# Kernel optimization log

Hardware: AMD Instinct MI355X
Metric: run time of the kernel (lower is better)

Reference implementation:

```python
import jax, jax.numpy as jnp
import numpy as np

N = 100000   # nodes
E = 1600000  # edges (no self loops; added per PyG default)
DIN = 64; DMID = 64; DOUT = 64; H = 8
C_MID = DMID // H  # per-head dim for concat layers
NEG_SLOPE = 0.2


def _segment_softmax(logits, seg, num):
    # logits: [E', H], seg: [E'] target node ids
    m = jax.ops.segment_max(logits, seg, num_segments=num)  # [N, H]
    e = jnp.exp(logits - m[seg])
    s = jax.ops.segment_sum(e, seg, num_segments=num)
    return e / (s[seg] + 1e-16)


def _gatv2_layer(x, src, dst, Wl, Wr, att, bias, heads, concat):
    n = x.shape[0]
    c = Wl.shape[1] // heads
    xl = (x @ Wl).reshape(n, heads, c)  # source transform
    xr = (x @ Wr).reshape(n, heads, c)  # target transform
    m = xl[src] + xr[dst]               # [E', H, C] gathered messages
    e = jnp.where(m > 0, m, NEG_SLOPE * m)
    alpha = jnp.einsum('ehc,hc->eh', e, att)            # [E', H]
    alpha = _segment_softmax(alpha, dst, n)
    out = jax.ops.segment_sum(alpha[..., None] * xl[src], dst, num_segments=n)  # [N, H, C]
    if concat:
        out = out.reshape(n, heads * c)
    else:
        out = out.mean(axis=1)
    return out + bias


def setup_inputs() -> dict:
    key = jax.random.key(0)
    ks = jax.random.split(key, 16)
    x = jax.random.normal(ks[0], (N, DIN), jnp.float32)
    src = jax.random.randint(ks[1], (E,), 0, N)
    dst = jax.random.randint(ks[2], (E,), 0, N)
    dst = jnp.where(src == dst, (dst + 1) % N, dst)  # no pre-existing self loops
    edge_index = jnp.stack([src, dst]).astype(jnp.int64)

    def lin(k, fi, fo):
        return jax.random.normal(k, (fi, fo), jnp.float32) / np.sqrt(fi)

    inp = {'x': x, 'edge_index': edge_index}
    # layer 0: din -> H*C_MID (concat), layer 1: dmid -> H*C_MID (concat), layer 2: dmid -> H*DOUT (mean)
    dims = [(DIN, H * C_MID, C_MID), (DMID, H * C_MID, C_MID), (DMID, H * DOUT, DOUT)]
    kidx = 3
    for i, (fi, fo, c) in enumerate(dims):
        inp[f'W{i}l'] = lin(ks[kidx], fi, fo); kidx += 1
        inp[f'W{i}r'] = lin(ks[kidx], fi, fo); kidx += 1
        inp[f'a{i}'] = jax.random.normal(ks[kidx], (H, c), jnp.float32) / np.sqrt(c); kidx += 1
        bsize = fo if i < 2 else DOUT
        inp[f'b{i}'] = jnp.zeros((bsize,), jnp.float32)
    return inp


def reference(x, edge_index, W0l, W0r, a0, b0, W1l, W1r, a1, b1, W2l, W2r, a2, b2):
    # add self loops (PyG GATv2Conv default add_self_loops=True)
    loop = jnp.arange(N, dtype=edge_index.dtype)
    src = jnp.concatenate([edge_index[0], loop])
    dst = jnp.concatenate([edge_index[1], loop])

    # eval mode: dropout is identity
    h = jax.nn.elu(_gatv2_layer(x, src, dst, W0l, W0r, a0, b0, H, True))
    prev_h = jnp.zeros_like(h)

    h_in = h + prev_h
    h = jax.nn.elu(_gatv2_layer(h_in, src, dst, W1l, W1r, a1, b1, H, True))
    prev_h = h_in

    h_in = h + prev_h
    out = _gatv2_layer(h_in, src, dst, W2l, W2r, a2, b2, H, False)
    return out
```

## Files before the change

kernel.cpp:

```cpp
#include <hip/hip_runtime.h>
#include <math.h>

#define NNODES 100000
typedef unsigned short bf16_t;

typedef __attribute__((ext_vector_type(8))) short bf16x8;
typedef __attribute__((ext_vector_type(4))) float f32x4;

__device__ __forceinline__ float bf_lo(unsigned u) { return __uint_as_float(u << 16); }
__device__ __forceinline__ float bf_hi(unsigned u) { return __uint_as_float(u & 0xffff0000u); }
__device__ __forceinline__ bf16_t f2bf(float f) {
  unsigned u = __float_as_uint(f);
  return (bf16_t)((u + 0x7fffu + ((u >> 16) & 1u)) >> 16);
}
__device__ __forceinline__ float leaky(float v) { return fmaxf(v, 0.2f * v); }

#define LDK 68

__global__ __launch_bounds__(256) void gemm_mfma(const float* __restrict__ in,
                                                 const float* __restrict__ Wl,
                                                 const float* __restrict__ Wr,
                                                 bf16_t* __restrict__ XL,
                                                 bf16_t* __restrict__ XR,
                                                 int n, int fo, int col0, int ncols) {
  __shared__ bf16_t sX[64][LDK];
  __shared__ bf16_t sL[64][LDK];
  __shared__ bf16_t sR[64][LDK];
  int r0 = blockIdx.x * 64;
  int ct = blockIdx.y * 64;
  for (int i = threadIdx.x; i < 64 * 64; i += 256) {
    int r = i >> 6, k = i & 63;
    float v = (r0 + r < n) ? in[(size_t)(r0 + r) * 64 + k] : 0.f;
    sX[r][k] = f2bf(v);
  }
  for (int i = threadIdx.x; i < 64 * 64; i += 256) {
    int k = i >> 6, c = i & 63;
    int gc = col0 + ct + c;
    sL[c][k] = f2bf(Wl[k * fo + gc]);
    sR[c][k] = f2bf(Wr[k * fo + gc]);
  }
  __syncthreads();
  int w = threadIdx.x >> 6, l = threadIdx.x & 63;
  int l16 = l & 15, kg = l >> 4;
  bf16x8 a0 = *(const bf16x8*)&sX[w * 16 + l16][kg * 8];
  bf16x8 a1 = *(const bf16x8*)&sX[w * 16 + l16][kg * 8 + 32];
  f32x4 accL[4], accR[4];
#pragma unroll
  for (int nt = 0; nt < 4; ++nt) {
#pragma unroll
    for (int r = 0; r < 4; ++r) { accL[nt][r] = 0.f; accR[nt][r] = 0.f; }
  }
#pragma unroll
  for (int nt = 0; nt < 4; ++nt) {
    bf16x8 bl0 = *(const bf16x8*)&sL[nt * 16 + l16][kg * 8];
    bf16x8 bl1 = *(const bf16x8*)&sL[nt * 16 + l16][kg * 8 + 32];
    bf16x8 br0 = *(const bf16x8*)&sR[nt * 16 + l16][kg * 8];
    bf16x8 br1 = *(const bf16x8*)&sR[nt * 16 + l16][kg * 8 + 32];
    accL[nt] = __builtin_amdgcn_mfma_f32_16x16x32_bf16(a0, bl0, accL[nt], 0, 0, 0);
    accL[nt] = __builtin_amdgcn_mfma_f32_16x16x32_bf16(a1, bl1, accL[nt], 0, 0, 0);
    accR[nt] = __builtin_amdgcn_mfma_f32_16x16x32_bf16(a0, br0, accR[nt], 0, 0, 0);
    accR[nt] = __builtin_amdgcn_mfma_f32_16x16x32_bf16(a1, br1, accR[nt], 0, 0, 0);
  }
#pragma unroll
  for (int nt = 0; nt < 4; ++nt) {
#pragma unroll
    for (int r = 0; r < 4; ++r) {
      int grow = r0 + w * 16 + kg * 4 + r;
      if (grow < n) {
        size_t o = (size_t)grow * ncols + ct + nt * 16 + l16;
        XL[o] = f2bf(accL[nt][r]);
        XR[o] = f2bf(accR[nt][r]);
      }
    }
  }
}

__global__ void zeroi(int* __restrict__ p, int n) {
  int i = blockIdx.x * blockDim.x + threadIdx.x;
  if (i < n) p[i] = 0;
}
__global__ void histrank(const int* __restrict__ ei, int E,
                         int* __restrict__ cnt, unsigned char* __restrict__ rank) {
  int e = blockIdx.x * blockDim.x + threadIdx.x;
  if (e < E) rank[e] = (unsigned char)atomicAdd(&cnt[ei[E + e]], 1);
}
__global__ void scan1(const int* __restrict__ cnt, int n,
                      int* __restrict__ scn, int* __restrict__ bsum) {
  __shared__ int sh[256];
  int t = threadIdx.x, i = blockIdx.x * 256 + t;
  int v = (i < n) ? cnt[i] : 0;
  sh[t] = v;
  __syncthreads();
  for (int off = 1; off < 256; off <<= 1) {
    int x = (t >= off) ? sh[t - off] : 0;
    __syncthreads();
    sh[t] += x;
    __syncthreads();
  }
  if (i < n) scn[i] = sh[t];
  if (t == 255) bsum[blockIdx.x] = sh[255];
}
__global__ void scan2(int* __restrict__ bsum, int nb) {
  __shared__ int sh[512];
  int t = threadIdx.x;
  sh[t] = (t < nb) ? bsum[t] : 0;
  __syncthreads();
  for (int off = 1; off < 512; off <<= 1) {
    int x = (t >= off) ? sh[t - off] : 0;
    __syncthreads();
    sh[t] += x;
    __syncthreads();
  }
  if (t < nb) bsum[t] = sh[t];
}
__global__ void scan3(int* __restrict__ RS, const int* __restrict__ bsum, int n) {
  int i = blockIdx.x * blockDim.x + threadIdx.x;
  if (i >= n) return;
  int b = i >> 8;
  int pre = (b > 0) ? bsum[b - 1] : 0;
  RS[i + 1] += pre;
  if (i == 0) RS[0] = 0;
}
__global__ void scat2(const int* __restrict__ ei, int E,
                      const int* __restrict__ RS,
                      const unsigned char* __restrict__ rank,
                      int* __restrict__ SRC) {
  int e = blockIdx.x * blockDim.x + threadIdx.x;
  if (e >= E) return;
  int d = ei[E + e];
  SRC[RS[d] + (int)rank[e]] = ei[e];
}

__global__ __launch_bounds__(256) void fused01(const bf16_t* __restrict__ xl,
                                               const bf16_t* __restrict__ xr,
                                               const float* __restrict__ att,
                                               const int* __restrict__ RS,
                                               const int* __restrict__ SRC,
                                               const float* __restrict__ bias,
                                               float* __restrict__ curbuf,
                                               int n, int addres) {
  int l = threadIdx.x & 63;
  int q = l & 15;
  int d = blockIdx.x * 16 + ((threadIdx.x >> 6) << 2) + (l >> 4);
  int dd = (d < n) ? d : 0;
  float a0 = att[4 * q], a1 = att[4 * q + 1], a2 = att[4 * q + 2], a3 = att[4 * q + 3];
  uint2 ur = ((const uint2*)xr)[(size_t)dd * 16 + q];
  float r0 = bf_lo(ur.x), r1 = bf_hi(ur.x), r2 = bf_lo(ur.y), r3 = bf_hi(ur.y);
  int rs = RS[dd], re = RS[dd + 1];
  int cnt = (d < n) ? (re - rs + 1) : 0;
  int mc = max(cnt, __shfl_xor(cnt, 16));
  mc = max(mc, __shfl_xor(mc, 32));
  float m = -1e30f, s = 0.f, ac0 = 0.f, ac1 = 0.f, ac2 = 0.f, ac3 = 0.f;
  int nsid = (rs < re) ? SRC[rs] : dd;
  uint2 u = ((const uint2*)xl)[(size_t)dd * 16 + q];
  for (int j = 0;;) {
    uint2 un = ((const uint2*)xl)[(size_t)nsid * 16 + q];
    int i2 = rs + j + 1;
    int nn = (i2 < re) ? SRC[i2] : dd;
    float x0 = bf_lo(u.x), x1 = bf_hi(u.x), x2 = bf_lo(u.y), x3 = bf_hi(u.y);
    float t = leaky(x0 + r0) * a0 + leaky(x1 + r1) * a1 +
              leaky(x2 + r2) * a2 + leaky(x3 + r3) * a3;
    t += __shfl_xor(t, 1);
    if (j >= cnt) t = -1e30f;
    if (__any(t > m + 8.f)) {
      float nm = fmaxf(m, t);
      float e0 = __expf(m - nm);
      s *= e0; ac0 *= e0; ac1 *= e0; ac2 *= e0; ac3 *= e0; m = nm;
    }
    float e1 = __expf(t - m);
    s += e1;
    ac0 += e1 * x0; ac1 += e1 * x1; ac2 += e1 * x2; ac3 += e1 * x3;
    ++j;
    if (j >= mc) break;
    u = un;
    nsid = nn;
  }
  if (d < n) {
    float inv = 1.f / (s + 1e-16f);
    float v0 = ac0 * inv + bias[4 * q];
    float v1 = ac1 * inv + bias[4 * q + 1];
    float v2 = ac2 * inv + bias[4 * q + 2];
    float v3 = ac3 * inv + bias[4 * q + 3];
    v0 = v0 > 0.f ? v0 : expm1f(v0);
    v1 = v1 > 0.f ? v1 : expm1f(v1);
    v2 = v2 > 0.f ? v2 : expm1f(v2);
    v3 = v3 > 0.f ? v3 : expm1f(v3);
    float4* pc = (float4*)(curbuf + (size_t)d * 64 + 4 * q);
    if (addres) {
      float4 pr = *pc;
      v0 += pr.x; v1 += pr.y; v2 += pr.z; v3 += pr.w;
    }
    *pc = make_float4(v0, v1, v2, v3);
  }
}

__global__ __launch_bounds__(256) void fused2(const bf16_t* __restrict__ xl,
                                              const bf16_t* __restrict__ xr,
                                              const float* __restrict__ att,
                                              const int* __restrict__ RS,
                                              const int* __restrict__ SRC,
                                              const float* __restrict__ bias,
                                              float* __restrict__ accbuf,
                                              float* __restrict__ outbuf,
                                              int n, int h0, int pass) {
  int l = threadIdx.x & 63;
  int ll = l & 31;
  int d = blockIdx.x * 8 + ((threadIdx.x >> 6) << 1) + (l >> 5);
  int dd = (d < n) ? d : 0;
  int h = ll >> 3, c0 = (ll & 7) * 8;
  const float* ap = att + (h0 + h) * 64 + c0;
  float a[8];
#pragma unroll
  for (int k = 0; k < 8; ++k) a[k] = ap[k];
  uint4 ur = ((const uint4*)xr)[(size_t)dd * 32 + ll];
  float r[8] = {bf_lo(ur.x), bf_hi(ur.x), bf_lo(ur.y), bf_hi(ur.y),
                bf_lo(ur.z), bf_hi(ur.z), bf_lo(ur.w), bf_hi(ur.w)};
  int rs = RS[dd], re = RS[dd + 1];
  int cnt = (d < n) ? (re - rs + 1) : 0;
  int maxcnt = max(cnt, __shfl_xor(cnt, 32));
  float m = -1e30f, s = 0.f;
  float ac[8] = {0.f, 0.f, 0.f, 0.f, 0.f, 0.f, 0.f, 0.f};
  int nsid = (rs < re) ? SRC[rs] : dd;
  uint4 u = ((const uint4*)xl)[(size_t)dd * 32 + ll];
  for (int j = 0;;) {
    uint4 un = ((const uint4*)xl)[(size_t)nsid * 32 + ll];
    int i2 = rs + j + 1;
    int nn = (i2 < re) ? SRC[i2] : dd;
    float x[8] = {bf_lo(u.x), bf_hi(u.x), bf_lo(u.y), bf_hi(u.y),
                  bf_lo(u.z), bf_hi(u.z), bf_lo(u.w), bf_hi(u.w)};
    float t = 0.f;
#pragma unroll
    for (int k = 0; k < 8; ++k) t += leaky(x[k] + r[k]) * a[k];
    t += __shfl_xor(t, 1);
    t += __shfl_xor(t, 2);
    t += __shfl_xor(t, 4);
    if (j >= cnt) t = -1e30f;
    if (__any(t > m + 8.f)) {
      float nm = fmaxf(m, t);
      float e0 = __expf(m - nm);
      s *= e0;
#pragma unroll
      for (int k = 0; k < 8; ++k) ac[k] *= e0;
      m = nm;
    }
    float e1 = __expf(t - m);
    s += e1;
#pragma unroll
    for (int k = 0; k < 8; ++k) ac[k] += e1 * x[k];
    ++j;
    if (j >= maxcnt) break;
    u = un;
    nsid = nn;
  }
  float inv = 1.f / (s + 1e-16f);
  float v[8];
#pragma unroll
  for (int k = 0; k < 8; ++k) {
    v[k] = ac[k] * inv;
    v[k] += __shfl_xor(v[k], 8);
    v[k] += __shfl_xor(v[k], 16);
  }
  if (ll < 8 && d < n) {
    float* pa = accbuf + (size_t)d * 64 + ll * 8;
    if (pass == 0) {
      *(float4*)pa = make_float4(v[0], v[1], v[2], v[3]);
      *(float4*)(pa + 4) = make_float4(v[4], v[5], v[6], v[7]);
    } else {
      float4 p0 = *(float4*)pa;
      float4 p1 = *(float4*)(pa + 4);
      const float* bp = bias + ll * 8;
      float4 o0, o1;
      o0.x = (p0.x + v[0]) * 0.125f + bp[0];
      o0.y = (p0.y + v[1]) * 0.125f + bp[1];
      o0.z = (p0.z + v[2]) * 0.125f + bp[2];
      o0.w = (p0.w + v[3]) * 0.125f + bp[3];
      o1.x = (p1.x + v[4]) * 0.125f + bp[4];
      o1.y = (p1.y + v[5]) * 0.125f + bp[5];
      o1.z = (p1.z + v[6]) * 0.125f + bp[6];
      o1.w = (p1.w + v[7]) * 0.125f + bp[7];
      float* po = outbuf + (size_t)d * 64 + ll * 8;
      *(float4*)po = o0;
      *(float4*)(po + 4) = o1;
    }
  }
}

extern "C" void kernel_launch(void* const* d_in, const int* in_sizes, int n_in,
                              void* d_out, int out_size, void* d_ws, size_t ws_size,
                              hipStream_t stream) {
  const float* x = (const float*)d_in[0];
  const int* ei = (const int*)d_in[1];
  const float* Wmat[3][2] = {
      {(const float*)d_in[2], (const float*)d_in[3]},
      {(const float*)d_in[6], (const float*)d_in[7]},
      {(const float*)d_in[10], (const float*)d_in[11]}};
  const float* att[3] = {(const float*)d_in[4], (const float*)d_in[8],
                         (const float*)d_in[12]};
  const float* bias[3] = {(const float*)d_in[5], (const float*)d_in[9],
                          (const float*)d_in[13]};
  const int N = NNODES;
  int E = in_sizes[1] / 2;

  char* p = (char*)d_ws;
  auto alloc = [&](size_t bytes) {
    char* r = p;
    p += (bytes + 255) & ~(size_t)255;
    return r;
  };
  float* CUR = (float*)alloc((size_t)N * 64 * 4);
  float* ACC = (float*)alloc((size_t)N * 64 * 4);
  bf16_t* XL = (bf16_t*)alloc((size_t)N * 256 * 2);
  bf16_t* XR = (bf16_t*)alloc((size_t)N * 256 * 2);
  int* RS = (int*)alloc((size_t)(N + 1) * 4);
  int* CNT = (int*)alloc((size_t)N * 4);
  int* BSUM = (int*)alloc(512 * 4);
  int* SRC = (int*)alloc((size_t)E * 4);
  unsigned char* RANK = (unsigned char*)alloc((size_t)E);

  const int nb = (N + 255) / 256;
  const int geblk = (E + 255) / 256;
  const int g01 = (N + 15) / 16;
  const int g2 = (N + 7) / 8;
  const int gx64 = (N + 63) / 64;

  zeroi<<<nb, 256, 0, stream>>>(CNT, N);
  histrank<<<geblk, 256, 0, stream>>>(ei, E, CNT, RANK);
  scan1<<<nb, 256, 0, stream>>>(CNT, N, RS + 1, BSUM);
  scan2<<<1, 512, 0, stream>>>(BSUM, nb);
  scan3<<<nb, 256, 0, stream>>>(RS, BSUM, N);
  scat2<<<geblk, 256, 0, stream>>>(ei, E, RS, RANK, SRC);

  for (int layer = 0; layer < 2; ++layer) {
    const float* in = (layer == 0) ? x : CUR;
    gemm_mfma<<<dim3(gx64, 1), 256, 0, stream>>>(in, Wmat[layer][0], Wmat[layer][1],
                                                 XL, XR, N, 64, 0, 64);
    fused01<<<g01, 256, 0, stream>>>(XL, XR, att[layer], RS, SRC, bias[layer],
                                     CUR, N, layer);
  }

  for (int hb = 0; hb < 2; ++hb) {
    gemm_mfma<<<dim3(gx64, 4), 256, 0, stream>>>(CUR, Wmat[2][0], Wmat[2][1],
                                                 XL, XR, N, 512, hb * 256, 256);
    fused2<<<g2, 256, 0, stream>>>(XL, XR, att[2], RS, SRC, bias[2],
                                   ACC, (float*)d_out, N, hb * 4, hb);
  }
}
```

Before: 622.7 us.

## Process all eight heads of final layer in one pass; use exp2 softmax

When the workspace is large enough, the final layer computes all eight heads' XL/XR tables with a single GEMM and one fused aggregation. Each node is then handled by a full wavefront, so the CSR traversal and the ACC round-trip happen once instead of twice. The attention vectors are prescaled by log2(e) so the online softmax can use exp2f, and byte-offset addressing with 32-bit indices replaces the size_t indexing. The trade-off is larger XL/XR tables, which increases the gather footprint and cache pressure, and one node per wavefront may lower latency hiding for low-degree nodes.

```diff
diff --git a/kernel.cpp b/kernel.cpp
--- a/kernel.cpp
+++ b/kernel.cpp
@@ -6,6 +6,9 @@
 
 typedef __attribute__((ext_vector_type(8))) short bf16x8;
 typedef __attribute__((ext_vector_type(4))) float f32x4;
+
+#define LOG2E 1.44269504f
+#define THR2 11.5415603f
 
 __device__ __forceinline__ float bf_lo(unsigned u) { return __uint_as_float(u << 16); }
 __device__ __forceinline__ float bf_hi(unsigned u) { return __uint_as_float(u & 0xffff0000u); }
@@ -143,8 +146,10 @@
   int q = l & 15;
   int d = blockIdx.x * 16 + ((threadIdx.x >> 6) << 2) + (l >> 4);
   int dd = (d < n) ? d : 0;
-  float a0 = att[4 * q], a1 = att[4 * q + 1], a2 = att[4 * q + 2], a3 = att[4 * q + 3];
-  uint2 ur = ((const uint2*)xr)[(size_t)dd * 16 + q];
+  float a0 = att[4 * q] * LOG2E, a1 = att[4 * q + 1] * LOG2E;
+  float a2 = att[4 * q + 2] * LOG2E, a3 = att[4 * q + 3] * LOG2E;
+  const char* xlb = (const char*)xl;
+  uint2 ur = *(const uint2*)((const char*)xr + ((unsigned)dd << 7) + (q << 3));
   float r0 = bf_lo(ur.x), r1 = bf_hi(ur.x), r2 = bf_lo(ur.y), r3 = bf_hi(ur.y);
   int rs = RS[dd], re = RS[dd + 1];
   int cnt = (d < n) ? (re - rs + 1) : 0;
@@ -152,9 +157,9 @@
   mc = max(mc, __shfl_xor(mc, 32));
   float m = -1e30f, s = 0.f, ac0 = 0.f, ac1 = 0.f, ac2 = 0.f, ac3 = 0.f;
   int nsid = (rs < re) ? SRC[rs] : dd;
-  uint2 u = ((const uint2*)xl)[(size_t)dd * 16 + q];
+  uint2 u = *(const uint2*)(xlb + ((unsigned)dd << 7) + (q << 3));
   for (int j = 0;;) {
-    uint2 un = ((const uint2*)xl)[(size_t)nsid * 16 + q];
+    uint2 un = *(const uint2*)(xlb + ((unsigned)nsid << 7) + (q << 3));
     int i2 = rs + j + 1;
     int nn = (i2 < re) ? SRC[i2] : dd;
     float x0 = bf_lo(u.x), x1 = bf_hi(u.x), x2 = bf_lo(u.y), x3 = bf_hi(u.y);
@@ -162,12 +167,12 @@
               leaky(x2 + r2) * a2 + leaky(x3 + r3) * a3;
     t += __shfl_xor(t, 1);
     if (j >= cnt) t = -1e30f;
-    if (__any(t > m + 8.f)) {
+    if (__any(t > m + THR2)) {
       float nm = fmaxf(m, t);
-      float e0 = __expf(m - nm);
+      float e0 = exp2f(m - nm);
       s *= e0; ac0 *= e0; ac1 *= e0; ac2 *= e0; ac3 *= e0; m = nm;
     }
-    float e1 = __expf(t - m);
+    float e1 = exp2f(t - m);
     s += e1;
     ac0 += e1 * x0; ac1 += e1 * x1; ac2 += e1 * x2; ac3 += e1 * x3;
     ++j;
@@ -194,6 +199,7 @@
   }
 }
 
+template <int NH>
 __global__ __launch_bounds__(256) void fused2(const bf16_t* __restrict__ xl,
                                               const bf16_t* __restrict__ xr,
                                               const float* __restrict__ att,
@@ -203,27 +209,31 @@
                                               float* __restrict__ accbuf,
                                               float* __restrict__ outbuf,
                                               int n, int h0, int pass) {
+  const int LPD = NH * 8;
+  const unsigned RB = NH * 128u;
   int l = threadIdx.x & 63;
-  int ll = l & 31;
-  int d = blockIdx.x * 8 + ((threadIdx.x >> 6) << 1) + (l >> 5);
+  int ll = l & (LPD - 1);
+  int d = blockIdx.x * (256 / LPD) + (threadIdx.x >> 6) * (64 / LPD) +
+          (NH == 4 ? (l >> 5) : 0);
   int dd = (d < n) ? d : 0;
   int h = ll >> 3, c0 = (ll & 7) * 8;
   const float* ap = att + (h0 + h) * 64 + c0;
   float a[8];
 #pragma unroll
-  for (int k = 0; k < 8; ++k) a[k] = ap[k];
-  uint4 ur = ((const uint4*)xr)[(size_t)dd * 32 + ll];
+  for (int k = 0; k < 8; ++k) a[k] = ap[k] * LOG2E;
+  const char* xlb = (const char*)xl;
+  uint4 ur = *(const uint4*)((const char*)xr + (unsigned)dd * RB + (ll << 4));
   float r[8] = {bf_lo(ur.x), bf_hi(ur.x), bf_lo(ur.y), bf_hi(ur.y),
                 bf_lo(ur.z), bf_hi(ur.z), bf_lo(ur.w), bf_hi(ur.w)};
   int rs = RS[dd], re = RS[dd + 1];
   int cnt = (d < n) ? (re - rs + 1) : 0;
-  int maxcnt = max(cnt, __shfl_xor(cnt, 32));
+  int maxcnt = (NH == 4) ? max(cnt, __shfl_xor(cnt, 32)) : cnt;
   float m = -1e30f, s = 0.f;
   float ac[8] = {0.f, 0.f, 0.f, 0.f, 0.f, 0.f, 0.f, 0.f};
   int nsid = (rs < re) ? SRC[rs] : dd;
-  uint4 u = ((const uint4*)xl)[(size_t)dd * 32 + ll];
+  uint4 u = *(const uint4*)(xlb + (unsigned)dd * RB + (ll << 4));
   for (int j = 0;;) {
-    uint4 un = ((const uint4*)xl)[(size_t)nsid * 32 + ll];
+    uint4 un = *(const uint4*)(xlb + (unsigned)nsid * RB + (ll << 4));
     int i2 = rs + j + 1;
     int nn = (i2 < re) ? SRC[i2] : dd;
     float x[8] = {bf_lo(u.x), bf_hi(u.x), bf_lo(u.y), bf_hi(u.y),
@@ -235,15 +245,15 @@
     t += __shfl_xor(t, 2);
     t += __shfl_xor(t, 4);
     if (j >= cnt) t = -1e30f;
-    if (__any(t > m + 8.f)) {
+    if (__any(t > m + THR2)) {
       float nm = fmaxf(m, t);
-      float e0 = __expf(m - nm);
+      float e0 = exp2f(m - nm);
       s *= e0;
 #pragma unroll
       for (int k = 0; k < 8; ++k) ac[k] *= e0;
       m = nm;
     }
-    float e1 = __expf(t - m);
+    float e1 = exp2f(t - m);
     s += e1;
 #pragma unroll
     for (int k = 0; k < 8; ++k) ac[k] += e1 * x[k];
@@ -259,28 +269,45 @@
     v[k] = ac[k] * inv;
     v[k] += __shfl_xor(v[k], 8);
     v[k] += __shfl_xor(v[k], 16);
+    if (NH == 8) v[k] += __shfl_xor(v[k], 32);
   }
   if (ll < 8 && d < n) {
-    float* pa = accbuf + (size_t)d * 64 + ll * 8;
-    if (pass == 0) {
-      *(float4*)pa = make_float4(v[0], v[1], v[2], v[3]);
-      *(float4*)(pa + 4) = make_float4(v[4], v[5], v[6], v[7]);
-    } else {
-      float4 p0 = *(float4*)pa;
-      float4 p1 = *(float4*)(pa + 4);
+    if (NH == 8) {
       const float* bp = bias + ll * 8;
       float4 o0, o1;
-      o0.x = (p0.x + v[0]) * 0.125f + bp[0];
-      o0.y = (p0.y + v[1]) * 0.125f + bp[1];
-      o0.z = (p0.z + v[2]) * 0.125f + bp[2];
-      o0.w = (p0.w + v[3]) * 0.125f + bp[3];
-      o1.x = (p1.x + v[4]) * 0.125f + bp[4];
-      o1.y = (p1.y + v[5]) * 0.125f + bp[5];
-      o1.z = (p1.z + v[6]) * 0.125f + bp[6];
-      o1.w = (p1.w + v[7]) * 0.125f + bp[7];
+      o0.x = v[0] * 0.125f + bp[0];
+      o0.y = v[1] * 0.125f + bp[1];
+      o0.z = v[2] * 0.125f + bp[2];
+      o0.w = v[3] * 0.125f + bp[3];
+      o1.x = v[4] * 0.125f + bp[4];
+      o1.y = v[5] * 0.125f + bp[5];
+      o1.z = v[6] * 0.125f + bp[6];
+      o1.w = v[7] * 0.125f + bp[7];
       float* po = outbuf + (size_t)d * 64 + ll * 8;
       *(float4*)po = o0;
       *(float4*)(po + 4) = o1;
+    } else {
+      float* pa = accbuf + (size_t)d * 64 + ll * 8;
+      if (pass == 0) {
+        *(float4*)pa = make_float4(v[0], v[1], v[2], v[3]);
+        *(float4*)(pa + 4) = make_float4(v[4], v[5], v[6], v[7]);
+      } else {
+        float4 p0 = *(float4*)pa;
+        float4 p1 = *(float4*)(pa + 4);
+        const float* bp = bias + ll * 8;
+        float4 o0, o1;
+        o0.x = (p0.x + v[0]) * 0.125f + bp[0];
+        o0.y = (p0.y + v[1]) * 0.125f + bp[1];
+        o0.z = (p0.z + v[2]) * 0.125f + bp[2];
+        o0.w = (p0.w + v[3]) * 0.125f + bp[3];
+        o1.x = (p1.x + v[4]) * 0.125f + bp[4];
+        o1.y = (p1.y + v[5]) * 0.125f + bp[5];
+        o1.z = (p1.z + v[6]) * 0.125f + bp[6];
+        o1.w = (p1.w + v[7]) * 0.125f + bp[7];
+        float* po = outbuf + (size_t)d * 64 + ll * 8;
+        *(float4*)po = o0;
+        *(float4*)(po + 4) = o1;
+      }
     }
   }
 }
@@ -301,6 +328,12 @@
   const int N = NNODES;
   int E = in_sizes[1] / 2;
 
+  auto al = [](size_t b) { return (b + 255) & ~(size_t)255; };
+  size_t csr_bytes = al((size_t)(N + 1) * 4) + al((size_t)N * 4) + al(512 * 4) +
+                     al((size_t)E * 4) + al((size_t)E);
+  size_t need8 = al((size_t)N * 64 * 4) + 2 * al((size_t)N * 512 * 2) + csr_bytes;
+  bool mode8 = (ws_size >= need8);
+
   char* p = (char*)d_ws;
   auto alloc = [&](size_t bytes) {
     char* r = p;
@@ -308,19 +341,19 @@
     return r;
   };
   float* CUR = (float*)alloc((size_t)N * 64 * 4);
-  float* ACC = (float*)alloc((size_t)N * 64 * 4);
-  bf16_t* XL = (bf16_t*)alloc((size_t)N * 256 * 2);
-  bf16_t* XR = (bf16_t*)alloc((size_t)N * 256 * 2);
+  size_t xtab = mode8 ? (size_t)N * 512 * 2 : (size_t)N * 256 * 2;
+  bf16_t* XL = (bf16_t*)alloc(xtab);
+  bf16_t* XR = (bf16_t*)alloc(xtab);
   int* RS = (int*)alloc((size_t)(N + 1) * 4);
   int* CNT = (int*)alloc((size_t)N * 4);
   int* BSUM = (int*)alloc(512 * 4);
   int* SRC = (int*)alloc((size_t)E * 4);
   unsigned char* RANK = (unsigned char*)alloc((size_t)E);
+  float* ACC = mode8 ? nullptr : (float*)alloc((size_t)N * 64 * 4);
 
   const int nb = (N + 255) / 256;
   const int geblk = (E + 255) / 256;
   const int g01 = (N + 15) / 16;
-  const int g2 = (N + 7) / 8;
   const int gx64 = (N + 63) / 64;
 
   zeroi<<<nb, 256, 0, stream>>>(CNT, N);
@@ -338,10 +371,17 @@
                                      CUR, N, layer);
   }
 
-  for (int hb = 0; hb < 2; ++hb) {
-    gemm_mfma<<<dim3(gx64, 4), 256, 0, stream>>>(CUR, Wmat[2][0], Wmat[2][1],
-                                                 XL, XR, N, 512, hb * 256, 256);
-    fused2<<<g2, 256, 0, stream>>>(XL, XR, att[2], RS, SRC, bias[2],
-                                   ACC, (float*)d_out, N, hb * 4, hb);
-  }
-}
+  if (mode8) {
+    gemm_mfma<<<dim3(gx64, 8), 256, 0, stream>>>(CUR, Wmat[2][0], Wmat[2][1],
+                                                 XL, XR, N, 512, 0, 512);
+    fused2<8><<<(N + 3) / 4, 256, 0, stream>>>(XL, XR, att[2], RS, SRC, bias[2],
+                                               nullptr, (float*)d_out, N, 0, 0);
+  } else {
+    for (int hb = 0; hb < 2; ++hb) {
+      gemm_mfma<<<dim3(gx64, 4), 256, 0, stream>>>(CUR, Wmat[2][0], Wmat[2][1],
+                                                   XL, XR, N, 512, hb * 256, 256);
+      fused2<4><<<(N + 7) / 8, 256, 0, stream>>>(XL, XR, att[2], RS, SRC, bias[2],
+                                                 ACC, (float*)d_out, N, hb * 4, hb);
+    }
+  }
+}
```

Measured after the change: 632.2 us. About the same (+1.5%).
